# Optimization experiments

Hardware: AMD Instinct MI355X
Metric: run time of the kernel (lower is better)

## Reference

```python
import jax, jax.numpy as jnp
import numpy as np

N_NODES = 100000
N_EDGES = 1600000
D_IN = 128
D_H = 128
N_LAYERS = 3
N_OUT = 10
N_GRAPHS = 64


def setup_inputs() -> dict:
    key = jax.random.key(0)
    ks = jax.random.split(key, 12)
    glorot = lambda k, fi, fo: jax.random.normal(k, (fi, fo), jnp.float32) * np.sqrt(2.0 / (fi + fo))
    return {
        "x": jax.random.normal(ks[0], (N_NODES, D_IN), jnp.float32),
        "edge_index": jax.random.randint(ks[1], (2, N_EDGES), 0, N_NODES, jnp.int64 if jax.config.jax_enable_x64 else jnp.int32),
        "batch": jnp.sort(jax.random.randint(ks[2], (N_NODES,), 0, N_GRAPHS)),
        "target_size": N_GRAPHS,
        "W1": glorot(ks[3], D_IN, D_H), "b1": jnp.zeros((D_H,), jnp.float32),
        "W2": glorot(ks[4], D_H, D_H), "b2": jnp.zeros((D_H,), jnp.float32),
        "W3": glorot(ks[5], D_H, D_H), "b3": jnp.zeros((D_H,), jnp.float32),
        "lin1_w": glorot(ks[6], N_LAYERS * D_H, D_H), "lin1_b": jnp.zeros((D_H,), jnp.float32),
        "lin2_w": glorot(ks[7], D_H, N_OUT), "lin2_b": jnp.zeros((N_OUT,), jnp.float32),
    }


def _gcn_conv(x, src, dst, norm, W, b, n_nodes):
    # PyG GCNConv: h = X W; out[dst] += norm * h[src]; out += b
    h = x @ W
    msg = h[src] * norm[:, None]            # [E+N, D_H] gathered messages
    out = jax.ops.segment_sum(msg, dst, num_segments=n_nodes)
    return out + b


def reference(x, edge_index, batch, target_size, W1, b1, W2, b2, W3, b3,
              lin1_w, lin1_b, lin2_w, lin2_b):
    n = x.shape[0]
    loops = jnp.arange(n, dtype=edge_index.dtype)
    src = jnp.concatenate([edge_index[0], loops])   # add self-loops (PyG default)
    dst = jnp.concatenate([edge_index[1], loops])
    deg = jax.ops.segment_sum(jnp.ones_like(src, dtype=x.dtype), dst, num_segments=n)
    dinv = jnp.where(deg > 0, jax.lax.rsqrt(deg), 0.0)
    norm = dinv[src] * dinv[dst]                    # symmetric normalization

    h1 = jax.nn.relu(_gcn_conv(x, src, dst, norm, W1, b1, n))
    h2 = jax.nn.relu(_gcn_conv(h1, src, dst, norm, W2, b2, n))
    h3 = jax.nn.relu(_gcn_conv(h2, src, dst, norm, W3, b3, n))
    h = jnp.concatenate([h1, h2, h3], axis=-1)      # JumpingKnowledge 'cat' -> [N, 3*D_H]

    # global_mean_pool over graphs
    counts = jax.ops.segment_sum(jnp.ones((n,), x.dtype), batch, num_segments=target_size)
    pooled = jax.ops.segment_sum(h, batch, num_segments=target_size)
    pooled = pooled / jnp.maximum(counts, 1.0)[:, None]

    g = jax.nn.relu(pooled @ lin1_w + lin1_b)       # dropout is identity at inference
    logits = g @ lin2_w + lin2_b
    return jax.nn.log_softmax(logits, axis=-1)
```

## Files before the change

### kernel.cpp

```cpp
#include <hip/hip_runtime.h>

#define NN 100000
#define NE 1600000
#define DH 128
#define NG 64

#define NBUCKU 98
#define EPB 4096
#define NBLK_BIN 391
#define CAP 20480

#define LDH 136
#define LDF 132

typedef __attribute__((ext_vector_type(2))) _Float16 half2v;
typedef __attribute__((ext_vector_type(4))) _Float16 half4;
typedef __attribute__((ext_vector_type(8))) _Float16 half8;
typedef __attribute__((ext_vector_type(4))) float f32x4;

__device__ inline unsigned int enc8(_Float16 h) {
  unsigned short b = __builtin_bit_cast(unsigned short, h);
  unsigned short r = (unsigned short)(b + 0x7F + ((b >> 8) & 1));
  return (unsigned int)(r >> 8);
}
__device__ inline half2v d02(unsigned int u) {
  return __builtin_bit_cast(half2v, (u << 8) & 0xFF00FF00u);
}
__device__ inline half2v d13(unsigned int u) {
  return __builtin_bit_cast(half2v, u & 0xFF00FF00u);
}

#define DEC4(u)                                                                         \
  acc[0] += d02(u.x); acc[1] += d13(u.x); acc[2] += d02(u.y); acc[3] += d13(u.y);       \
  acc[4] += d02(u.z); acc[5] += d13(u.z); acc[6] += d02(u.w); acc[7] += d13(u.w);

__device__ inline void gather_rows(const unsigned char* __restrict__ bp,
                                   const int* __restrict__ csr_src,
                                   int p, int e, half2v (&acc)[8]) {
  if (p + 3 < e) {
    int j0 = csr_src[p], j1 = csr_src[p + 1], j2 = csr_src[p + 2], j3 = csr_src[p + 3];
    uint4 c0 = *(const uint4*)(bp + (size_t)j0 * DH);
    uint4 c1 = *(const uint4*)(bp + (size_t)j1 * DH);
    uint4 c2 = *(const uint4*)(bp + (size_t)j2 * DH);
    uint4 c3 = *(const uint4*)(bp + (size_t)j3 * DH);
    p += 4;
    int pb = (p + 3 < e) ? p : p - 4;
    j0 = csr_src[pb]; j1 = csr_src[pb + 1]; j2 = csr_src[pb + 2]; j3 = csr_src[pb + 3];
    while (p + 3 < e) {
      uint4 n0 = *(const uint4*)(bp + (size_t)j0 * DH);
      uint4 n1 = *(const uint4*)(bp + (size_t)j1 * DH);
      uint4 n2 = *(const uint4*)(bp + (size_t)j2 * DH);
      uint4 n3 = *(const uint4*)(bp + (size_t)j3 * DH);
      p += 4;
      int pb2 = (p + 3 < e) ? p : p - 4;
      j0 = csr_src[pb2]; j1 = csr_src[pb2 + 1]; j2 = csr_src[pb2 + 2]; j3 = csr_src[pb2 + 3];
      DEC4(c0); DEC4(c1); DEC4(c2); DEC4(c3);
      c0 = n0; c1 = n1; c2 = n2; c3 = n3;
    }
    DEC4(c0); DEC4(c1); DEC4(c2); DEC4(c3);
  }
  for (; p < e; ++p) {
    uint4 u0 = *(const uint4*)(bp + (size_t)csr_src[p] * DH);
    DEC4(u0);
  }
}


__global__ __launch_bounds__(256) void k_build(const int* __restrict__ esrc,
                                               const int* __restrict__ edst,
                                               const int* __restrict__ batch,
                                               const float* __restrict__ W0,
                                               const float* __restrict__ W1,
                                               const float* __restrict__ W2,
                                               int* __restrict__ bucketCursor,
                                               unsigned int* __restrict__ pairs,
                                               int* __restrict__ startg,
                                               _Float16* __restrict__ Wt) {
  int b = blockIdx.x, t = threadIdx.x;
  int gtid = b * 256 + t;

  if (gtid < 3 * DH * DH) {
    int l = gtid >> 14;
    int rem = gtid & 16383;
    int n = rem >> 7, k = rem & 127;
    const float* W = (l == 0) ? W0 : (l == 1) ? W1 : W2;
    Wt[(size_t)l * DH * DH + n * DH + k] = (_Float16)W[k * DH + n];
  }
  if (gtid < NN) {
    int bat = batch[gtid];
    int prev = (gtid == 0) ? -1 : batch[gtid - 1];
    for (int g = prev + 1; g <= bat; ++g) startg[g] = gtid;
    if (gtid == NN - 1)
      for (int g = bat + 1; g <= NG; ++g) startg[g] = NN;
  }

  __shared__ int h[NBUCKU];
  __shared__ int cur[NBUCKU];
  if (t < NBUCKU) h[t] = 0;
  __syncthreads();
  int base = b * EPB;
  int dv[EPB / 256];
#pragma unroll
  for (int i = 0; i < EPB / 256; ++i) {
    int e = base + i * 256 + t;
    dv[i] = (e < NE) ? edst[e] : -1;
    if (e < NE) atomicAdd(&h[dv[i] >> 10], 1);
  }
  __syncthreads();
  if (t < NBUCKU) {
    int rel = atomicAdd(&bucketCursor[t], h[t]);
    cur[t] = t * CAP + rel;
  }
  __syncthreads();
#pragma unroll
  for (int i = 0; i < EPB / 256; ++i) {
    int e = base + i * 256 + t;
    if (e < NE) {
      int d = dv[i];
      int q = atomicAdd(&cur[d >> 10], 1);
      pairs[q] = ((unsigned int)esrc[e] << 10) | (unsigned int)(d & 1023);
    }
  }
}


__global__ __launch_bounds__(256) void k_finalize(const unsigned int* __restrict__ pairs,
                                                  const int* __restrict__ bucketCursor,
                                                  int* __restrict__ offA,
                                                  int* __restrict__ offB,
                                                  float* __restrict__ dinv,
                                                  int* __restrict__ csr_src) {
  __shared__ int cnt[1024];
  __shared__ int tsum[256];
  int b = blockIdx.x, t = threadIdx.x;
  int nodeBase = b << 10;
  for (int i = t; i < 1024; i += 256) cnt[i] = 0;
  __syncthreads();
  int pStart = b * CAP;
  int pEnd = pStart + bucketCursor[b];
  for (int p = pStart + t; p < pEnd; p += 256)
    atomicAdd(&cnt[pairs[p] & 1023], 1);
  __syncthreads();
  int c0 = cnt[t * 4], c1 = cnt[t * 4 + 1], c2 = cnt[t * 4 + 2], c3 = cnt[t * 4 + 3];
  tsum[t] = c0 + c1 + c2 + c3;
  __syncthreads();
  for (int off = 1; off < 256; off <<= 1) {
    int v = (t >= off) ? tsum[t - off] : 0;
    __syncthreads();
    tsum[t] += v;
    __syncthreads();
  }
  int basep = pStart + ((t > 0) ? tsum[t - 1] : 0);
  int e0 = basep, e1 = basep + c0, e2 = e1 + c1, e3 = e2 + c2;
  __syncthreads();
  cnt[t * 4] = e0; cnt[t * 4 + 1] = e1; cnt[t * 4 + 2] = e2; cnt[t * 4 + 3] = e3;
  int g = nodeBase + t * 4;
  if (g < NN)     { offA[g] = e0;     offB[g] = e1;      dinv[g] = rsqrtf((float)c0 + 1.f); }
  if (g + 1 < NN) { offA[g + 1] = e1; offB[g + 1] = e2;  dinv[g + 1] = rsqrtf((float)c1 + 1.f); }
  if (g + 2 < NN) { offA[g + 2] = e2; offB[g + 2] = e3;  dinv[g + 2] = rsqrtf((float)c2 + 1.f); }
  if (g + 3 < NN) { offA[g + 3] = e3; offB[g + 3] = e3 + c3; dinv[g + 3] = rsqrtf((float)c3 + 1.f); }
  __syncthreads();
  for (int p = pStart + t; p < pEnd; p += 256) {
    unsigned int pr = pairs[p];
    int pos = atomicAdd(&cnt[pr & 1023], 1);
    csr_src[pos] = (int)(pr >> 10);
  }
}


template <bool F32IN>
__global__ __launch_bounds__(256) void k_gemm(const void* __restrict__ Ap,
                                              const _Float16* __restrict__ Wt,
                                              const float* __restrict__ dinv,
                                              unsigned char* __restrict__ Out8) {
  __shared__ _Float16 Wl[128 * LDH];
  int tid = threadIdx.x;
  int rowBase = blockIdx.x * 128;

#pragma unroll
  for (int i = 0; i < 8; ++i) {
    int chunk = tid + i * 256;
    int r = chunk >> 4, c = (chunk & 15) * 8;
    *(half8*)&Wl[r * LDH + c] = *(const half8*)(Wt + r * DH + c);
  }

  int wv = tid >> 6;
  int lane = tid & 63;
  int n16 = lane & 15;
  int quad = lane >> 4;

  int r0 = rowBase + wv * 32 + n16;
  int r1 = r0 + 16;

  half8 af[2][4];
  if (F32IN) {
    const float* A = (const float*)Ap;
#pragma unroll
    for (int kk = 0; kk < 4; ++kk) {
      half8 z = {};
      if (r0 < NN) {
        float4 lo = *(const float4*)(A + (size_t)r0 * DH + quad * 8 + kk * 32);
        float4 hi = *(const float4*)(A + (size_t)r0 * DH + quad * 8 + kk * 32 + 4);
        z = (half8){(_Float16)lo.x, (_Float16)lo.y, (_Float16)lo.z, (_Float16)lo.w,
                    (_Float16)hi.x, (_Float16)hi.y, (_Float16)hi.z, (_Float16)hi.w};
      }
      af[0][kk] = z;
      half8 z1 = {};
      if (r1 < NN) {
        float4 lo = *(const float4*)(A + (size_t)r1 * DH + quad * 8 + kk * 32);
        float4 hi = *(const float4*)(A + (size_t)r1 * DH + quad * 8 + kk * 32 + 4);
        z1 = (half8){(_Float16)lo.x, (_Float16)lo.y, (_Float16)lo.z, (_Float16)lo.w,
                     (_Float16)hi.x, (_Float16)hi.y, (_Float16)hi.z, (_Float16)hi.w};
      }
      af[1][kk] = z1;
    }
  } else {
    const _Float16* A = (const _Float16*)Ap;
#pragma unroll
    for (int kk = 0; kk < 4; ++kk) {
      half8 z = {};
      if (r0 < NN) z = *(const half8*)(A + (size_t)r0 * DH + quad * 8 + kk * 32);
      af[0][kk] = z;
      half8 z1 = {};
      if (r1 < NN) z1 = *(const half8*)(A + (size_t)r1 * DH + quad * 8 + kk * 32);
      af[1][kk] = z1;
    }
  }
  __syncthreads();

  f32x4 acc[2][8];
#pragma unroll
  for (int mt = 0; mt < 2; ++mt)
#pragma unroll
    for (int ct = 0; ct < 8; ++ct) acc[mt][ct] = (f32x4){0.f, 0.f, 0.f, 0.f};

  const _Float16* bp = &Wl[n16 * LDH + quad * 8];
#pragma unroll
  for (int kk = 0; kk < 4; ++kk) {
#pragma unroll
    for (int ct = 0; ct < 8; ++ct) {
      half8 bf = *(const half8*)(bp + (size_t)ct * 16 * LDH + kk * 32);
      acc[0][ct] = __builtin_amdgcn_mfma_f32_16x16x32_f16(af[0][kk], bf, acc[0][ct], 0, 0, 0);
      acc[1][ct] = __builtin_amdgcn_mfma_f32_16x16x32_f16(af[1][kk], bf, acc[1][ct], 0, 0, 0);
    }
  }

  float dv[2][4];
#pragma unroll
  for (int mt = 0; mt < 2; ++mt)
#pragma unroll
    for (int r = 0; r < 4; ++r) {
      int gr = rowBase + wv * 32 + mt * 16 + quad * 4 + r;
      dv[mt][r] = (gr < NN) ? dinv[gr] : 0.f;
    }

  __syncthreads();
#pragma unroll
  for (int mt = 0; mt < 2; ++mt)
#pragma unroll
    for (int ct = 0; ct < 8; ++ct)
#pragma unroll
      for (int r = 0; r < 4; ++r)
        Wl[(wv * 32 + mt * 16 + quad * 4 + r) * LDH + ct * 16 + n16] =
            (_Float16)(acc[mt][ct][r] * dv[mt][r]);
  __syncthreads();

#pragma unroll
  for (int i = 0; i < 8; ++i) {
    int chunk = tid + i * 256;
    int r = chunk >> 4, c = (chunk & 15) * 8;
    int gr = rowBase + r;
    if (gr < NN) {
      half8 v = *(const half8*)&Wl[r * LDH + c];
      unsigned int lo = enc8(v[0]) | (enc8(v[1]) << 8) | (enc8(v[2]) << 16) | (enc8(v[3]) << 24);
      unsigned int hi = enc8(v[4]) | (enc8(v[5]) << 8) | (enc8(v[6]) << 16) | (enc8(v[7]) << 24);
      uint2 st = {lo, hi};
      *(uint2*)(Out8 + (size_t)gr * DH + c) = st;
    }
  }
}


__global__ __launch_bounds__(512) void k_fused(const unsigned char* __restrict__ hs8_in,
                                               const int* __restrict__ csr_src,
                                               const int* __restrict__ offA,
                                               const int* __restrict__ offB,
                                               const float* __restrict__ dinv,
                                               const float* __restrict__ bias,
                                               const int* __restrict__ batch,
                                               const int* __restrict__ startg,
                                               float* __restrict__ pooled,
                                               int colOff,
                                               const _Float16* __restrict__ Wt,
                                               unsigned char* __restrict__ hs8_out) {
  __shared__ _Float16 Hl[64 * LDH];
  __shared__ _Float16 Wl[128 * LDH];
  int tid = threadIdx.x;
  int n0 = blockIdx.x * 64;

#pragma unroll
  for (int i = 0; i < 4; ++i) {
    int chunk = tid + i * 512;
    int r = chunk >> 4, c = (chunk & 15) * 8;
    *(half8*)&Wl[r * LDH + c] = *(const half8*)(Wt + r * DH + c);
  }

  int nd = tid >> 3;
  int part = tid & 7;
  int n = n0 + nd;
  bool valid = (n < NN);

  half2v acc[8];
#pragma unroll
  for (int i = 0; i < 8; ++i) acc[i] = (half2v){(_Float16)0, (_Float16)0};

  if (valid) {
    const unsigned char* bp = hs8_in + part * 16;
    uint4 us = *(const uint4*)(bp + (size_t)n * DH);
    DEC4(us);
    gather_rows(bp, csr_src, offA[n], offB[n], acc);
  }

  float dv = valid ? dinv[n] : 0.f;
#pragma unroll
  for (int w = 0; w < 4; ++w) {
    int dim = part * 16 + w * 4;
    float4 b4 = *(const float4*)(bias + dim);
    float h0 = valid ? fmaxf(fmaf((float)acc[2 * w][0], dv, b4.x), 0.f) : 0.f;
    float h1 = valid ? fmaxf(fmaf((float)acc[2 * w + 1][0], dv, b4.y), 0.f) : 0.f;
    float h2 = valid ? fmaxf(fmaf((float)acc[2 * w][1], dv, b4.z), 0.f) : 0.f;
    float h3 = valid ? fmaxf(fmaf((float)acc[2 * w + 1][1], dv, b4.w), 0.f) : 0.f;
    half4 hh = {(_Float16)h0, (_Float16)h1, (_Float16)h2, (_Float16)h3};
    *(half4*)&Hl[nd * LDH + dim] = hh;
  }
  __syncthreads();

  if (tid < DH) {
    int nEnd = (n0 + 64 < NN) ? n0 + 64 : NN;
    int gF = batch[n0];
    int gL = batch[nEnd - 1];
    for (int g = gF; g <= gL; ++g) {
      int rs = (startg[g] > n0) ? startg[g] : n0;
      int re = (startg[g + 1] < nEnd) ? startg[g + 1] : nEnd;
      if (re > rs) {
        float sum = 0.f;
        for (int r2 = rs; r2 < re; ++r2) sum += (float)Hl[(r2 - n0) * LDH + tid];
        atomicAdd(&pooled[g * (3 * DH) + colOff + tid], sum);
      }
    }
  }

  int wv = tid >> 6;
  int lane = tid & 63;
  int n16 = lane & 15;
  int quad = lane >> 4;
  int m16 = wv >> 1;
  int ctB = (wv & 1) * 4;

  f32x4 acc2[4];
#pragma unroll
  for (int ct = 0; ct < 4; ++ct) acc2[ct] = (f32x4){0.f, 0.f, 0.f, 0.f};

  const _Float16* ap = &Hl[(m16 * 16 + n16) * LDH + quad * 8];
#pragma unroll
  for (int kk = 0; kk < 4; ++kk) {
    half8 af = *(const half8*)(ap + kk * 32);
#pragma unroll
    for (int ct = 0; ct < 4; ++ct) {
      half8 bf = *(const half8*)&Wl[((ctB + ct) * 16 + n16) * LDH + quad * 8 + kk * 32];
      acc2[ct] = __builtin_amdgcn_mfma_f32_16x16x32_f16(af, bf, acc2[ct], 0, 0, 0);
    }
  }

  float dvo[4];
#pragma unroll
  for (int rr = 0; rr < 4; ++rr) {
    int gr = n0 + m16 * 16 + quad * 4 + rr;
    dvo[rr] = (gr < NN) ? dinv[gr] : 0.f;
  }

  __syncthreads();
#pragma unroll
  for (int ct = 0; ct < 4; ++ct)
#pragma unroll
    for (int rr = 0; rr < 4; ++rr)
      Hl[(m16 * 16 + quad * 4 + rr) * LDH + (ctB + ct) * 16 + n16] =
          (_Float16)(acc2[ct][rr] * dvo[rr]);
  __syncthreads();

#pragma unroll
  for (int i = 0; i < 2; ++i) {
    int chunk = tid + i * 512;
    int r = chunk >> 4, c = (chunk & 15) * 8;
    int gr = n0 + r;
    if (gr < NN) {
      half8 v = *(const half8*)&Hl[r * LDH + c];
      unsigned int lo = enc8(v[0]) | (enc8(v[1]) << 8) | (enc8(v[2]) << 16) | (enc8(v[3]) << 24);
      unsigned int hi = enc8(v[4]) | (enc8(v[5]) << 8) | (enc8(v[6]) << 16) | (enc8(v[7]) << 24);
      uint2 st = {lo, hi};
      *(uint2*)(hs8_out + (size_t)gr * DH + c) = st;
    }
  }
}


__global__ __launch_bounds__(512) void k_aggregate(const unsigned char* __restrict__ hs8,
                                                   const int* __restrict__ csr_src,
                                                   const int* __restrict__ offA,
                                                   const int* __restrict__ offB,
                                                   const float* __restrict__ dinv,
                                                   const float* __restrict__ bias,
                                                   const int* __restrict__ batch,
                                                   const int* __restrict__ startg,
                                                   float* __restrict__ pooled,
                                                   int colOff) {
  __shared__ float stage[64][LDF];
  int tid = threadIdx.x;
  int n0 = blockIdx.x * 64;
  int nd = tid >> 3;
  int part = tid & 7;
  int n = n0 + nd;
  bool valid = (n < NN);

  half2v acc[8];
#pragma unroll
  for (int i = 0; i < 8; ++i) acc[i] = (half2v){(_Float16)0, (_Float16)0};

  if (valid) {
    const unsigned char* bp = hs8 + part * 16;
    uint4 us = *(const uint4*)(bp + (size_t)n * DH);
    DEC4(us);
    gather_rows(bp, csr_src, offA[n], offB[n], acc);
  }

  float dv = valid ? dinv[n] : 0.f;
#pragma unroll
  for (int w = 0; w < 4; ++w) {
    int dim = part * 16 + w * 4;
    float4 b4 = *(const float4*)(bias + dim);
    float4 r;
    r.x = valid ? fmaxf(fmaf((float)acc[2 * w][0], dv, b4.x), 0.f) : 0.f;
    r.y = valid ? fmaxf(fmaf((float)acc[2 * w + 1][0], dv, b4.y), 0.f) : 0.f;
    r.z = valid ? fmaxf(fmaf((float)acc[2 * w][1], dv, b4.z), 0.f) : 0.f;
    r.w = valid ? fmaxf(fmaf((float)acc[2 * w + 1][1], dv, b4.w), 0.f) : 0.f;
    *(float4*)&stage[nd][dim] = r;
  }
  __syncthreads();

  if (tid < DH) {
    int nEnd = (n0 + 64 < NN) ? n0 + 64 : NN;
    int gF = batch[n0];
    int gL = batch[nEnd - 1];
    for (int g = gF; g <= gL; ++g) {
      int rs = (startg[g] > n0) ? startg[g] : n0;
      int re = (startg[g + 1] < nEnd) ? startg[g + 1] : nEnd;
      if (re > rs) {
        float sum = 0.f;
        for (int r2 = rs; r2 < re; ++r2) sum += stage[r2 - n0][tid];
        atomicAdd(&pooled[g * (3 * DH) + colOff + tid], sum);
      }
    }
  }
}


__global__ __launch_bounds__(128) void k_head(const float* __restrict__ pooled,
                                              const int* __restrict__ startg,
                                              const float* __restrict__ l1w,
                                              const float* __restrict__ l1b,
                                              const float* __restrict__ l2w,
                                              const float* __restrict__ l2b,
                                              float* __restrict__ out) {
  __shared__ float pr[3 * DH];
  __shared__ float grow[DH];
  __shared__ float lg[16];
  int g = blockIdx.x, t = threadIdx.x;
  float cnt = (float)(startg[g + 1] - startg[g]);
  float inv = 1.0f / fmaxf(cnt, 1.0f);
  for (int k = t; k < 3 * DH; k += 128) pr[k] = pooled[g * (3 * DH) + k] * inv;
  __syncthreads();
  float acc = l1b[t];
  for (int k = 0; k < 3 * DH; ++k) acc = fmaf(pr[k], l1w[k * DH + t], acc);
  grow[t] = fmaxf(acc, 0.f);
  __syncthreads();
  if (t < 10) {
    float a = l2b[t];
    for (int k = 0; k < DH; ++k) a = fmaf(grow[k], l2w[k * 10 + t], a);
    lg[t] = a;
  }
  __syncthreads();
  if (t < 10) {
    float m = lg[0];
    for (int i = 1; i < 10; ++i) m = fmaxf(m, lg[i]);
    float sum = 0.f;
    for (int i = 0; i < 10; ++i) sum += expf(lg[i] - m);
    out[g * 10 + t] = lg[t] - m - logf(sum);
  }
}


extern "C" void kernel_launch(void* const* d_in, const int* in_sizes, int n_in,
                              void* d_out, int out_size, void* d_ws, size_t ws_size,
                              hipStream_t stream) {
  const float* x = (const float*)d_in[0];
  const int* ei = (const int*)d_in[1];
  const int* esrc = ei;
  const int* edst = ei + NE;
  const int* batch = (const int*)d_in[2];
  const float* W0 = (const float*)d_in[4];
  const float* W1 = (const float*)d_in[6];
  const float* W2 = (const float*)d_in[8];
  const float* B[3] = {(const float*)d_in[5], (const float*)d_in[7], (const float*)d_in[9]};
  const float* l1w = (const float*)d_in[10];
  const float* l1b = (const float*)d_in[11];
  const float* l2w = (const float*)d_in[12];
  const float* l2b = (const float*)d_in[13];
  float* out = (float*)d_out;

  char* ws = (char*)d_ws;
  size_t off = 0;
  auto alloc = [&](size_t bytes) {
    char* p = ws + off;
    off = (off + bytes + 255) & ~(size_t)255;
    return p;
  };
  float* pooled = (float*)alloc((size_t)NG * 3 * DH * 4);
  int* bucketCursor = (int*)alloc(NBUCKU * 4);
  size_t msBytes = (size_t)NG * 3 * DH * 4 + 512;

  int* offA = (int*)alloc((size_t)NN * 4);
  int* offB = (int*)alloc((size_t)NN * 4);
  float* dinv = (float*)alloc((size_t)NN * 4);
  int* startg = (int*)alloc((NG + 1) * 4);
  _Float16* Wt = (_Float16*)alloc((size_t)3 * DH * DH * 2);
  unsigned char* hs8A = (unsigned char*)alloc((size_t)NN * DH);
  unsigned char* hs8B = (unsigned char*)alloc((size_t)NN * DH);
  unsigned int* pairs = (unsigned int*)alloc((size_t)NBUCKU * CAP * 4);
  int* csr_src = (int*)alloc((size_t)NBUCKU * CAP * 4);

  hipMemsetAsync(pooled, 0, msBytes, stream);

  k_build<<<NBLK_BIN, 256, 0, stream>>>(esrc, edst, batch, W0, W1, W2,
                                        bucketCursor, pairs, startg, Wt);
  k_finalize<<<NBUCKU, 256, 0, stream>>>(pairs, bucketCursor, offA, offB, dinv, csr_src);

  k_gemm<true><<<(NN + 127) / 128, 256, 0, stream>>>((const void*)x, Wt, dinv, hs8A);

  int nFusedBlk = (NN + 63) / 64;
  k_fused<<<nFusedBlk, 512, 0, stream>>>(hs8A, csr_src, offA, offB, dinv, B[0], batch,
                                         startg, pooled, 0,
                                         Wt + (size_t)1 * DH * DH, hs8B);
  k_fused<<<nFusedBlk, 512, 0, stream>>>(hs8B, csr_src, offA, offB, dinv, B[1], batch,
                                         startg, pooled, DH,
                                         Wt + (size_t)2 * DH * DH, hs8A);

  k_aggregate<<<nFusedBlk, 512, 0, stream>>>(hs8A, csr_src, offA, offB, dinv, B[2],
                                             batch, startg, pooled, 2 * DH);

  k_head<<<NG, 128, 0, stream>>>(pooled, startg, l1w, l1b, l2w, l2b, out);
}
```

Baseline: 335.9 us.

## Build CSR with global degree atomics, block-scan, and atomic placement

Replaces the two-pass bucketed CSR build (an LDS histogram into a bucket staging array, then a per-bucket finalize) with three kernels. The first counts in-degrees with global atomics, the second runs a block-wise scan whose block base comes from an atomic on a global cursor, and the third places each edge source via a per-node global atomic cursor. The weight transpose moves into a small separate kernel that goes through a shared-memory tile. This drops the intermediate pairs buffer and its extra read pass, but trades LDS atomics for about 3.2M contended global atomics and adds launches.

After: 473.0 us. 40.8% more time.

```diff
diff --git a/kernel.cpp b/kernel.cpp
--- a/kernel.cpp
+++ b/kernel.cpp
@@ -5,10 +5,8 @@
 #define DH 128
 #define NG 64
 
-#define NBUCKU 98
 #define EPB 4096
 #define NBLK_BIN 391
-#define CAP 20480
 
 #define LDH 136
 #define LDF 132
@@ -66,26 +64,35 @@
 }
 
 
-__global__ __launch_bounds__(256) void k_build(const int* __restrict__ esrc,
-                                               const int* __restrict__ edst,
-                                               const int* __restrict__ batch,
-                                               const float* __restrict__ W0,
-                                               const float* __restrict__ W1,
-                                               const float* __restrict__ W2,
-                                               int* __restrict__ bucketCursor,
-                                               unsigned int* __restrict__ pairs,
-                                               int* __restrict__ startg,
-                                               _Float16* __restrict__ Wt) {
+__global__ __launch_bounds__(256) void k_pre(const float* __restrict__ W0,
+                                             const float* __restrict__ W1,
+                                             const float* __restrict__ W2,
+                                             _Float16* __restrict__ Wt) {
+  __shared__ _Float16 tile[128][LDH];
+  int l = blockIdx.x, t = threadIdx.x;
+  const float* W = (l == 0) ? W0 : (l == 1) ? W1 : W2;
+#pragma unroll
+  for (int i = 0; i < 64; ++i) {
+    int idx = i * 256 + t;
+    int r = idx >> 7, c = idx & 127;
+    tile[c][r] = (_Float16)W[r * DH + c];
+  }
+  __syncthreads();
+#pragma unroll
+  for (int i = 0; i < 8; ++i) {
+    int idx = i * 256 + t;
+    int n = idx >> 4, c = (idx & 15) * 8;
+    *(half8*)&Wt[(size_t)l * DH * DH + n * DH + c] = *(const half8*)&tile[n][c];
+  }
+}
+
+
+__global__ __launch_bounds__(256) void k_deg(const int* __restrict__ edst,
+                                             const int* __restrict__ batch,
+                                             int* __restrict__ deg,
+                                             int* __restrict__ startg) {
   int b = blockIdx.x, t = threadIdx.x;
   int gtid = b * 256 + t;
-
-  if (gtid < 3 * DH * DH) {
-    int l = gtid >> 14;
-    int rem = gtid & 16383;
-    int n = rem >> 7, k = rem & 127;
-    const float* W = (l == 0) ? W0 : (l == 1) ? W1 : W2;
-    Wt[(size_t)l * DH * DH + n * DH + k] = (_Float16)W[k * DH + n];
-  }
   if (gtid < NN) {
     int bat = batch[gtid];
     int prev = (gtid == 0) ? -1 : batch[gtid - 1];
@@ -93,55 +100,29 @@
     if (gtid == NN - 1)
       for (int g = bat + 1; g <= NG; ++g) startg[g] = NN;
   }
-
-  __shared__ int h[NBUCKU];
-  __shared__ int cur[NBUCKU];
-  if (t < NBUCKU) h[t] = 0;
-  __syncthreads();
   int base = b * EPB;
-  int dv[EPB / 256];
 #pragma unroll
   for (int i = 0; i < EPB / 256; ++i) {
     int e = base + i * 256 + t;
-    dv[i] = (e < NE) ? edst[e] : -1;
-    if (e < NE) atomicAdd(&h[dv[i] >> 10], 1);
-  }
-  __syncthreads();
-  if (t < NBUCKU) {
-    int rel = atomicAdd(&bucketCursor[t], h[t]);
-    cur[t] = t * CAP + rel;
-  }
-  __syncthreads();
-#pragma unroll
-  for (int i = 0; i < EPB / 256; ++i) {
-    int e = base + i * 256 + t;
-    if (e < NE) {
-      int d = dv[i];
-      int q = atomicAdd(&cur[d >> 10], 1);
-      pairs[q] = ((unsigned int)esrc[e] << 10) | (unsigned int)(d & 1023);
-    }
-  }
-}
-
-
-__global__ __launch_bounds__(256) void k_finalize(const unsigned int* __restrict__ pairs,
-                                                  const int* __restrict__ bucketCursor,
-                                                  int* __restrict__ offA,
-                                                  int* __restrict__ offB,
-                                                  float* __restrict__ dinv,
-                                                  int* __restrict__ csr_src) {
-  __shared__ int cnt[1024];
+    if (e < NE) atomicAdd(&deg[edst[e]], 1);
+  }
+}
+
+
+__global__ __launch_bounds__(256) void k_scan(const int* __restrict__ deg,
+                                              int* __restrict__ gcur,
+                                              int* __restrict__ offA,
+                                              int* __restrict__ offB,
+                                              float* __restrict__ dinv,
+                                              int* __restrict__ cursor) {
   __shared__ int tsum[256];
+  __shared__ int sbase;
   int b = blockIdx.x, t = threadIdx.x;
-  int nodeBase = b << 10;
-  for (int i = t; i < 1024; i += 256) cnt[i] = 0;
-  __syncthreads();
-  int pStart = b * CAP;
-  int pEnd = pStart + bucketCursor[b];
-  for (int p = pStart + t; p < pEnd; p += 256)
-    atomicAdd(&cnt[pairs[p] & 1023], 1);
-  __syncthreads();
-  int c0 = cnt[t * 4], c1 = cnt[t * 4 + 1], c2 = cnt[t * 4 + 2], c3 = cnt[t * 4 + 3];
+  int g = (b << 10) + t * 4;
+  int c0 = (g < NN) ? deg[g] : 0;
+  int c1 = (g + 1 < NN) ? deg[g + 1] : 0;
+  int c2 = (g + 2 < NN) ? deg[g + 2] : 0;
+  int c3 = (g + 3 < NN) ? deg[g + 3] : 0;
   tsum[t] = c0 + c1 + c2 + c3;
   __syncthreads();
   for (int off = 1; off < 256; off <<= 1) {
@@ -150,20 +131,31 @@
     tsum[t] += v;
     __syncthreads();
   }
-  int basep = pStart + ((t > 0) ? tsum[t - 1] : 0);
-  int e0 = basep, e1 = basep + c0, e2 = e1 + c1, e3 = e2 + c2;
-  __syncthreads();
-  cnt[t * 4] = e0; cnt[t * 4 + 1] = e1; cnt[t * 4 + 2] = e2; cnt[t * 4 + 3] = e3;
-  int g = nodeBase + t * 4;
-  if (g < NN)     { offA[g] = e0;     offB[g] = e1;      dinv[g] = rsqrtf((float)c0 + 1.f); }
-  if (g + 1 < NN) { offA[g + 1] = e1; offB[g + 1] = e2;  dinv[g + 1] = rsqrtf((float)c1 + 1.f); }
-  if (g + 2 < NN) { offA[g + 2] = e2; offB[g + 2] = e3;  dinv[g + 2] = rsqrtf((float)c2 + 1.f); }
-  if (g + 3 < NN) { offA[g + 3] = e3; offB[g + 3] = e3 + c3; dinv[g + 3] = rsqrtf((float)c3 + 1.f); }
-  __syncthreads();
-  for (int p = pStart + t; p < pEnd; p += 256) {
-    unsigned int pr = pairs[p];
-    int pos = atomicAdd(&cnt[pr & 1023], 1);
-    csr_src[pos] = (int)(pr >> 10);
+  if (t == 255) sbase = atomicAdd(gcur, tsum[255]);
+  __syncthreads();
+  int basep = sbase + ((t > 0) ? tsum[t - 1] : 0);
+  int e0 = basep, e1 = e0 + c0, e2 = e1 + c1, e3 = e2 + c2;
+  if (g < NN)     { offA[g] = e0;     offB[g] = e1;     dinv[g] = rsqrtf((float)c0 + 1.f);     cursor[g] = e0; }
+  if (g + 1 < NN) { offA[g + 1] = e1; offB[g + 1] = e2; dinv[g + 1] = rsqrtf((float)c1 + 1.f); cursor[g + 1] = e1; }
+  if (g + 2 < NN) { offA[g + 2] = e2; offB[g + 2] = e3; dinv[g + 2] = rsqrtf((float)c2 + 1.f); cursor[g + 2] = e2; }
+  if (g + 3 < NN) { offA[g + 3] = e3; offB[g + 3] = e3 + c3; dinv[g + 3] = rsqrtf((float)c3 + 1.f); cursor[g + 3] = e3; }
+}
+
+
+__global__ __launch_bounds__(256) void k_place(const int* __restrict__ esrc,
+                                               const int* __restrict__ edst,
+                                               int* __restrict__ cursor,
+                                               int* __restrict__ csr_src) {
+  int b = blockIdx.x, t = threadIdx.x;
+  int base = b * EPB;
+#pragma unroll
+  for (int i = 0; i < EPB / 256; ++i) {
+    int e = base + i * 256 + t;
+    if (e < NE) {
+      int d = edst[e];
+      int pos = atomicAdd(&cursor[d], 1);
+      csr_src[pos] = esrc[e];
+    }
   }
 }
 
@@ -525,24 +517,26 @@
     return p;
   };
   float* pooled = (float*)alloc((size_t)NG * 3 * DH * 4);
-  int* bucketCursor = (int*)alloc(NBUCKU * 4);
-  size_t msBytes = (size_t)NG * 3 * DH * 4 + 512;
+  int* gcur = (int*)alloc(4);
+  int* deg = (int*)alloc((size_t)NN * 4);
+  size_t msBytes = 98304 + 256 + 400128;
 
   int* offA = (int*)alloc((size_t)NN * 4);
   int* offB = (int*)alloc((size_t)NN * 4);
   float* dinv = (float*)alloc((size_t)NN * 4);
+  int* cursor = (int*)alloc((size_t)NN * 4);
   int* startg = (int*)alloc((NG + 1) * 4);
   _Float16* Wt = (_Float16*)alloc((size_t)3 * DH * DH * 2);
   unsigned char* hs8A = (unsigned char*)alloc((size_t)NN * DH);
   unsigned char* hs8B = (unsigned char*)alloc((size_t)NN * DH);
-  unsigned int* pairs = (unsigned int*)alloc((size_t)NBUCKU * CAP * 4);
-  int* csr_src = (int*)alloc((size_t)NBUCKU * CAP * 4);
+  int* csr_src = (int*)alloc((size_t)NE * 4);
 
   hipMemsetAsync(pooled, 0, msBytes, stream);
 
-  k_build<<<NBLK_BIN, 256, 0, stream>>>(esrc, edst, batch, W0, W1, W2,
-                                        bucketCursor, pairs, startg, Wt);
-  k_finalize<<<NBUCKU, 256, 0, stream>>>(pairs, bucketCursor, offA, offB, dinv, csr_src);
+  k_pre<<<3, 256, 0, stream>>>(W0, W1, W2, Wt);
+  k_deg<<<NBLK_BIN, 256, 0, stream>>>(edst, batch, deg, startg);
+  k_scan<<<(NN + 1023) / 1024, 256, 0, stream>>>(deg, gcur, offA, offB, dinv, cursor);
+  k_place<<<NBLK_BIN, 256, 0, stream>>>(esrc, edst, cursor, csr_src);
 
   k_gemm<true><<<(NN + 127) / 128, 256, 0, stream>>>((const void*)x, Wt, dinv, hs8A);
 
```
